# Optimization experiments

Hardware: AMD Instinct MI355X
Metric: run time of the kernel (lower is better)

The kernel has to match this reference:

```python
import jax, jax.numpy as jnp
import numpy as np

_SQRT4PI = float(np.sqrt(4.0 * np.pi))

def spherical_harmonics_l2(vec):
    # e3nn real spherical harmonics, lmax=2, normalize=True, normalization='integral'
    # component-normalized values divided by sqrt(4*pi); e3nn (x,y,z) ordering with y as zenith
    r = jnp.linalg.norm(vec, axis=-1, keepdims=True)
    u = vec / jnp.maximum(r, 1e-12)
    x, y, z = u[..., 0], u[..., 1], u[..., 2]
    c1 = np.float32(np.sqrt(3.0)); c2 = np.float32(np.sqrt(15.0)); c3 = np.float32(np.sqrt(5.0))
    sh = jnp.stack([
        jnp.ones_like(x),                      # l=0
        c1 * x, c1 * y, c1 * z,                # l=1
        c2 * x * z,                            # l=2
        c2 * x * y,
        c3 * (y * y - 0.5 * (x * x + z * z)),
        c2 * y * z,
        (c2 * 0.5) * (z * z - x * x),
    ], axis=-1)
    return sh * np.float32(1.0 / _SQRT4PI)

def setup_inputs() -> dict:
    key = jax.random.key(0)
    ks = jax.random.split(key, 8)
    N, M, C, F, SH = 50000, 12, 128, 64, 9
    return dict(
        atom_fea=jax.random.normal(ks[0], (N, C), jnp.float32),
        nbr_fea=jax.random.normal(ks[1], (N, M, F), jnp.float32),
        nbr_idx=jax.random.randint(ks[2], (N, M), 0, N),
        pos=jax.random.normal(ks[3], (N, 3), jnp.float32),
        w1=jax.random.normal(ks[4], (F, F), jnp.float32) * np.float32(1.0 / np.sqrt(F)),
        b1=jnp.zeros((F,), jnp.float32),
        w2=jax.random.normal(ks[5], (F, SH), jnp.float32) * np.float32(1.0 / np.sqrt(F)),
        b2=jnp.zeros((SH,), jnp.float32),
        tp_w=jax.random.normal(ks[6], (C, C), jnp.float32),  # FCTP weight, path (Cx0e)x(1x0e)->(Cx0e)
        bn_gamma=jnp.ones((C,), jnp.float32),
        bn_beta=jnp.zeros((C,), jnp.float32),
    )

def reference(atom_fea, nbr_fea, nbr_idx, pos, w1, b1, w2, b2, tp_w, bn_gamma, bn_beta):
    N, M, F = nbr_fea.shape
    C = atom_fea.shape[1]
    src = nbr_idx.reshape(-1)                                  # (E,)
    h_j = atom_fea[src]                                        # (E, C) gather
    # radial MLP: Linear -> Softplus -> Linear
    R = jax.nn.softplus(nbr_fea.reshape(N * M, F) @ w1 + b1) @ w2 + b2   # (E, 9)
    rel = pos[src] - jnp.repeat(pos, M, axis=0)                # (E, 3), dst = arange(N) repeated M times
    Y = spherical_harmonics_l2(rel)                            # (E, 9)
    W = R * Y                                                  # (E, 9)
    # FullyConnectedTensorProduct(Cx0e, 0e+1o+2e, Cx0e): only 0e x 0e -> 0e path survives,
    # fan-in normalization alpha = 1/sqrt(C)
    msg = (h_j @ tp_w) * W[:, :1] * np.float32(1.0 / np.sqrt(C))  # (E, C)
    # scatter-mean over dst: dst rows are contiguous blocks of size M per node
    agg = msg.reshape(N, M, C).mean(axis=1)                    # (N, C)
    x = atom_fea + agg
    # BatchNorm1d (training-mode batch statistics, eps=1e-5)
    mean = x.mean(axis=0)
    var = x.var(axis=0)
    xn = (x - mean) * jax.lax.rsqrt(var + 1e-5)
    return jax.nn.softplus(bn_gamma * xn + bn_beta)
```

## Files before the change

kernel.cpp:

```cpp
#include <hip/hip_runtime.h>
#include <hip/hip_bf16.h>
#include <cstddef>

#define N_NODES 50000
#define M_NBR   12
#define C_CH    128
#define F_DIM   64
#define E_EDGES (N_NODES * M_NBR)
#define NSUP    18750
#define NBLK_A  2344
#define NBLK_Y  782
#define NBLK_G  782

constexpr float SCALE_CE =
    (float)(1.0 / (3.5449077018110318 * 11.313708498984761 * 12.0));

typedef __bf16 bf16x8 __attribute__((ext_vector_type(8)));
typedef float  f32x4  __attribute__((ext_vector_type(4)));

__device__ __forceinline__ float softplus_f(float x) {
    const float t = __builtin_amdgcn_exp2f(-fabsf(x) * 1.44269504f);
    return fmaxf(x, 0.0f) + 0.69314718f * __builtin_amdgcn_logf(1.0f + t);
}

__device__ __forceinline__ float bfhi_to_f(unsigned int p) {
    return __uint_as_float(p & 0xffff0000u);
}
__device__ __forceinline__ float bflo_to_f(unsigned int p) {
    return __uint_as_float(p << 16);
}

__global__ __launch_bounds__(512) void kW(
    const float* __restrict__ w1,
    const float* __restrict__ tp_w,
    __bf16* __restrict__ fragW1,
    __bf16* __restrict__ fragTP)
{
    const int t = threadIdx.x;
    if (blockIdx.x == 0) {
        const int lane = t & 63;
        const int f = t >> 6;
        const int n = f >> 1, ks = f & 1;
        const int col16 = lane & 15, kgrp = lane >> 4;
        bf16x8 v;
        #pragma unroll
        for (int j = 0; j < 8; ++j)
            v[j] = (__bf16)w1[(ks * 32 + kgrp * 8 + j) * F_DIM + 16 * n + col16];
        *(bf16x8*)&fragW1[(size_t)t * 8] = v;
    } else {
        const int fid = (blockIdx.x - 1) * 512 + t;
        const int lane = fid & 63;
        const int f = fid >> 6;
        const int n = f >> 2, ks = f & 3;
        const int col16 = lane & 15, kgrp = lane >> 4;
        bf16x8 v;
        #pragma unroll
        for (int j = 0; j < 8; ++j)
            v[j] = (__bf16)tp_w[(ks * 32 + kgrp * 8 + j) * C_CH + 16 * n + col16];
        *(bf16x8*)&fragTP[(size_t)fid * 8] = v;
    }
}

__global__ __launch_bounds__(256) void kFront(
    const float* __restrict__ nbr_fea,
    const __bf16* __restrict__ fragW1,
    const float* __restrict__ b1,
    const float* __restrict__ w2,
    const float* __restrict__ b2,
    const float* __restrict__ atom_fea,
    const __bf16* __restrict__ fragTP,
    float* __restrict__ ce,
    __bf16* __restrict__ y)
{
    __shared__ __align__(16) unsigned char smem[4 * 32 * 272];
    const int tid   = threadIdx.x;
    const int lane  = tid & 63;
    const int wid   = tid >> 6;
    const int col16 = lane & 15;
    const int kgrp  = lane >> 4;

    if (blockIdx.x < NBLK_A) {
        bf16x8 bfrag[4][2];
        #pragma unroll
        for (int f = 0; f < 8; ++f)
            bfrag[f >> 1][f & 1] = *(const bf16x8*)&fragW1[((size_t)f * 64 + lane) * 8];

        float b1v[4], w2v[4];
        #pragma unroll
        for (int n = 0; n < 4; ++n) {
            b1v[n] = b1[16 * n + col16];
            w2v[n] = w2[(16 * n + col16) * 9];
        }
        const float b2_0 = b2[0];

        float* S = (float*)(smem + (size_t)wid * 32 * 272);
        const int sup_base = (blockIdx.x * 4 + wid) * 2;

        #pragma unroll
        for (int st = 0; st < 2; ++st) {
            const int sup = sup_base + st;
            if (sup >= NSUP) break;
            const long e0 = (long)sup * 32;
            const float* gsrc = nbr_fea + e0 * F_DIM;

            #pragma unroll
            for (int i = 0; i < 8; ++i) {
                const int gi16 = i * 64 + lane;
                const float4 v = *(const float4*)(gsrc + (size_t)gi16 * 4);
                const int row = gi16 >> 4;
                const int u   = gi16 & 15;
                *(float4*)(S + row * 68 + u * 4) = v;
            }

            #pragma unroll
            for (int t = 0; t < 2; ++t) {
                const float* R = S + (t * 16 + col16) * 68 + kgrp * 8;
                const float4 a0 = *(const float4*)(R);
                const float4 a1 = *(const float4*)(R + 4);
                const float4 a2 = *(const float4*)(R + 32);
                const float4 a3 = *(const float4*)(R + 36);

                bf16x8 afrag[2];
                afrag[0][0] = (__bf16)a0.x; afrag[0][1] = (__bf16)a0.y;
                afrag[0][2] = (__bf16)a0.z; afrag[0][3] = (__bf16)a0.w;
                afrag[0][4] = (__bf16)a1.x; afrag[0][5] = (__bf16)a1.y;
                afrag[0][6] = (__bf16)a1.z; afrag[0][7] = (__bf16)a1.w;
                afrag[1][0] = (__bf16)a2.x; afrag[1][1] = (__bf16)a2.y;
                afrag[1][2] = (__bf16)a2.z; afrag[1][3] = (__bf16)a2.w;
                afrag[1][4] = (__bf16)a3.x; afrag[1][5] = (__bf16)a3.y;
                afrag[1][6] = (__bf16)a3.z; afrag[1][7] = (__bf16)a3.w;

                f32x4 acc[4];
                #pragma unroll
                for (int n = 0; n < 4; ++n) acc[n] = (f32x4){0.f, 0.f, 0.f, 0.f};
                #pragma unroll
                for (int ks = 0; ks < 2; ++ks)
                    #pragma unroll
                    for (int n = 0; n < 4; ++n)
                        acc[n] = __builtin_amdgcn_mfma_f32_16x16x32_bf16(
                            afrag[ks], bfrag[n][ks], acc[n], 0, 0, 0);

                float partial[4] = {0.f, 0.f, 0.f, 0.f};
                #pragma unroll
                for (int n = 0; n < 4; ++n)
                    #pragma unroll
                    for (int r = 0; r < 4; ++r) {
                        const float h = acc[n][r] + b1v[n];
                        partial[r] = fmaf(softplus_f(h), w2v[n], partial[r]);
                    }
                #pragma unroll
                for (int r = 0; r < 4; ++r) {
                    #pragma unroll
                    for (int off = 1; off <= 8; off <<= 1)
                        partial[r] += __shfl_xor(partial[r], off);
                }
                if (col16 == 0) {
                    const long et = e0 + t * 16;
                    #pragma unroll
                    for (int r = 0; r < 4; ++r)
                        ce[et + kgrp * 4 + r] = (partial[r] + b2_0) * SCALE_CE;
                }
            }
        }
    } else {
        __bf16* yl = (__bf16*)smem;
        const int blk  = blockIdx.x - NBLK_A;
        const int row  = blk * 64 + wid * 16 + col16;
        const int rowc = row < N_NODES ? row : N_NODES - 1;
        const float* ap = atom_fea + (size_t)rowc * C_CH + kgrp * 8;

        bf16x8 afrag[4];
        #pragma unroll
        for (int ks = 0; ks < 4; ++ks) {
            float4 f0 = *(const float4*)(ap + ks * 32);
            float4 f1 = *(const float4*)(ap + ks * 32 + 4);
            afrag[ks][0] = (__bf16)f0.x; afrag[ks][1] = (__bf16)f0.y;
            afrag[ks][2] = (__bf16)f0.z; afrag[ks][3] = (__bf16)f0.w;
            afrag[ks][4] = (__bf16)f1.x; afrag[ks][5] = (__bf16)f1.y;
            afrag[ks][6] = (__bf16)f1.z; afrag[ks][7] = (__bf16)f1.w;
        }

        #pragma unroll
        for (int n = 0; n < 8; ++n) {
            f32x4 acc = (f32x4){0.f, 0.f, 0.f, 0.f};
            #pragma unroll
            for (int ks = 0; ks < 4; ++ks) {
                bf16x8 bf = *(const bf16x8*)&fragTP[((size_t)(n * 4 + ks) * 64 + lane) * 8];
                acc = __builtin_amdgcn_mfma_f32_16x16x32_bf16(afrag[ks], bf, acc, 0, 0, 0);
            }
            #pragma unroll
            for (int r = 0; r < 4; ++r)
                yl[(wid * 16 + kgrp * 4 + r) * 136 + 16 * n + col16] = (__bf16)acc[r];
        }
        __syncthreads();

        #pragma unroll
        for (int it = 0; it < 4; ++it) {
            const int e  = it * 2048 + tid * 8;
            const int rw = e >> 7, cl = e & 127;
            const int grow = blk * 64 + rw;
            if (grow < N_NODES) {
                bf16x8 v = *(const bf16x8*)&yl[rw * 136 + cl];
                *(bf16x8*)&y[(size_t)grow * C_CH + cl] = v;
            }
        }
    }
}

__global__ __launch_bounds__(256, 6) void kG(
    const float* __restrict__ atom_fea,
    const __bf16* __restrict__ y,
    const int*   __restrict__ nbr_idx,
    const float* __restrict__ ce,
    unsigned int* __restrict__ xb,
    float* __restrict__ psum,
    float* __restrict__ psumsq)
{
    __shared__ float4 red[4][64];
    const int tid  = threadIdx.x;
    const int lane = tid & 63;
    const int wid  = tid >> 6;
    const int blk  = blockIdx.x;
    const int i0   = blk * 64 + wid * 16;

    float2 sum   = make_float2(0.f, 0.f);
    float2 sumsq = make_float2(0.f, 0.f);

    int   pidx = 0;
    float pce  = 0.f;
    if (i0 < N_NODES && lane < M_NBR) {
        pidx = nbr_idx[i0 * M_NBR + lane];
        pce  = ce[i0 * M_NBR + lane];
    }

    for (int t = 0; t < 16; ++t) {
        const int i = i0 + t;
        const int   cidx = pidx;
        const float cce  = pce;
        const int inext = i + 1;
        if (t < 15 && inext < N_NODES && lane < M_NBR) {
            pidx = nbr_idx[inext * M_NBR + lane];
            pce  = ce[inext * M_NBR + lane];
        }
        if (i < N_NODES) {
            float2 acc = make_float2(0.f, 0.f);
            #pragma unroll
            for (int m = 0; m < M_NBR; ++m) {
                const int   src = __shfl(cidx, m);
                const float c   = __shfl(cce, m);
                const unsigned int p =
                    *(const unsigned int*)(y + (size_t)src * C_CH + lane * 2);
                acc.x = fmaf(c, bflo_to_f(p), acc.x);
                acc.y = fmaf(c, bfhi_to_f(p), acc.y);
            }
            const float2 a = *(const float2*)(atom_fea + (size_t)i * C_CH + lane * 2);
            const float2 xv = make_float2(a.x + acc.x, a.y + acc.y);
            union { __bf16 h[2]; unsigned int u; } pk;
            pk.h[0] = (__bf16)xv.x;
            pk.h[1] = (__bf16)xv.y;
            xb[(size_t)i * 64 + lane] = pk.u;
            sum.x += xv.x; sum.y += xv.y;
            sumsq.x += xv.x * xv.x; sumsq.y += xv.y * xv.y;
        }
    }

    red[wid][lane] = make_float4(sum.x, sum.y, sumsq.x, sumsq.y);
    __syncthreads();
    if (tid < 128) {
        const int l = tid >> 1, comp = tid & 1;
        float s = 0.f, q = 0.f;
        #pragma unroll
        for (int w = 0; w < 4; ++w) {
            const float4 v = red[w][l];
            s += comp ? v.y : v.x;
            q += comp ? v.w : v.z;
        }
        psum[blk * 128 + tid]   = s;
        psumsq[blk * 128 + tid] = q;
    }
}

__global__ __launch_bounds__(1024) void kC1(
    const float* __restrict__ psum,
    const float* __restrict__ psumsq,
    float* __restrict__ mean_o,
    float* __restrict__ istd_o,
    int nblocks)
{
    __shared__ float red[2][8][128];
    const int t = threadIdx.x;
    const int c = t & 127;
    const int grp = t >> 7;
    float s = 0.f, ss = 0.f;
    for (int b = grp; b < nblocks; b += 8) {
        s  += psum[b * 128 + c];
        ss += psumsq[b * 128 + c];
    }
    red[0][grp][c] = s;
    red[1][grp][c] = ss;
    __syncthreads();
    if (t < 128) {
        float S = 0.f, SS = 0.f;
        #pragma unroll
        for (int k = 0; k < 8; ++k) { S += red[0][k][t]; SS += red[1][k][t]; }
        const float m   = S / (float)N_NODES;
        const float var = SS / (float)N_NODES - m * m;
        mean_o[t] = m;
        istd_o[t] = rsqrtf(var + 1e-5f);
    }
}

__global__ __launch_bounds__(256) void kC2(
    const unsigned int* __restrict__ xb,
    float* __restrict__ out,
    const float* __restrict__ mean_i,
    const float* __restrict__ istd_i,
    const float* __restrict__ gamma,
    const float* __restrict__ beta)
{
    __shared__ float sm[128], si[128], sg[128], sb[128];
    const int tid = threadIdx.x;
    if (tid < 128) {
        sm[tid] = mean_i[tid];
        si[tid] = istd_i[tid];
        sg[tid] = gamma[tid];
        sb[tid] = beta[tid];
    }
    __syncthreads();
    const size_t tix = (size_t)blockIdx.x * 256 + tid;
    const uint2 v = *(const uint2*)&xb[tix * 2];
    const int c0 = (int)(tix & 31) * 4;
    float r[4] = {bflo_to_f(v.x), bfhi_to_f(v.x), bflo_to_f(v.y), bfhi_to_f(v.y)};
    float4 o;
    #pragma unroll
    for (int t = 0; t < 4; ++t) {
        const int cc = c0 + t;
        const float xn = (r[t] - sm[cc]) * si[cc];
        r[t] = softplus_f(fmaf(sg[cc], xn, sb[cc]));
    }
    o.x = r[0]; o.y = r[1]; o.z = r[2]; o.w = r[3];
    *(float4*)&out[tix * 4] = o;
}

extern "C" void kernel_launch(void* const* d_in, const int* in_sizes, int n_in,
                              void* d_out, int out_size, void* d_ws, size_t ws_size,
                              hipStream_t stream)
{
    const float* atom_fea = (const float*)d_in[0];
    const float* nbr_fea  = (const float*)d_in[1];
    const int*   nbr_idx  = (const int*)d_in[2];
    const float* w1       = (const float*)d_in[4];
    const float* b1       = (const float*)d_in[5];
    const float* w2       = (const float*)d_in[6];
    const float* b2       = (const float*)d_in[7];
    const float* tp_w     = (const float*)d_in[8];
    const float* bn_gamma = (const float*)d_in[9];
    const float* bn_beta  = (const float*)d_in[10];

    float* out = (float*)d_out;
    float* ws  = (float*)d_ws;

    float* ce      = ws;
    float* psum    = ce + E_EDGES;
    float* psumsq  = psum + (size_t)NBLK_G * 128;
    float* mean_b  = psumsq + (size_t)NBLK_G * 128;
    float* istd_b  = mean_b + 128;
    __bf16* fragW1 = (__bf16*)(istd_b + 128);
    __bf16* fragTP = fragW1 + 4096;
    __bf16* ybuf   = fragTP + 16384;
    unsigned int* xbuf = (unsigned int*)(ybuf + 6400000);

    kW<<<5, 512, 0, stream>>>(w1, tp_w, fragW1, fragTP);
    kFront<<<NBLK_A + NBLK_Y, 256, 0, stream>>>(
        nbr_fea, fragW1, b1, w2, b2, atom_fea, fragTP, ce, ybuf);
    kG<<<NBLK_G, 256, 0, stream>>>(atom_fea, ybuf, nbr_idx, ce,
                                   xbuf, psum, psumsq);
    kC1<<<1, 1024, 0, stream>>>(psum, psumsq, mean_b, istd_b, NBLK_G);
    const int nC2 = (N_NODES * C_CH / 4) / 256;
    kC2<<<nC2, 256, 0, stream>>>(xbuf, out, mean_b, istd_b, bn_gamma, bn_beta);
}
```

Measured before the change: 111.2 us.

## Prefetch nbr_fea in registers, stage bf16 in LDS, fuse BN reduction via last-block

The radial-MLP part of kFront now handles four 32-edge supertiles per wave and software-prefetches the next tile's nbr_fea into registers while the current one computes. Tiles are converted to bf16 before the LDS store, so A fragments become direct 16-byte vector loads and the LDS footprint shrinks. The separate kC1 reduction kernel is removed: kG uses an atomic counter with a last-block-done pattern to compute the batch-norm mean and inverse std, which saves one launch at the cost of a fence and an atomic per block. The counter is reset inside kFront, so correctness depends on stream ordering.

```diff
diff --git a/kernel.cpp b/kernel.cpp
--- a/kernel.cpp
+++ b/kernel.cpp
@@ -8,7 +8,8 @@
 #define F_DIM   64
 #define E_EDGES (N_NODES * M_NBR)
 #define NSUP    18750
-#define NBLK_A  2344
+#define SUP_PER_WAVE 4
+#define NBLK_A  1172
 #define NBLK_Y  782
 #define NBLK_G  782
 
@@ -70,15 +71,18 @@
     const float* __restrict__ atom_fea,
     const __bf16* __restrict__ fragTP,
     float* __restrict__ ce,
-    __bf16* __restrict__ y)
-{
-    __shared__ __align__(16) unsigned char smem[4 * 32 * 272];
+    __bf16* __restrict__ y,
+    unsigned int* __restrict__ counter)
+{
+    __shared__ __align__(16) unsigned char smem[18432];
     const int tid   = threadIdx.x;
     const int lane  = tid & 63;
     const int wid   = tid >> 6;
     const int col16 = lane & 15;
     const int kgrp  = lane >> 4;
 
+    if (blockIdx.x == 0 && tid == 0) *counter = 0;
+
     if (blockIdx.x < NBLK_A) {
         bf16x8 bfrag[4][2];
         #pragma unroll
@@ -93,42 +97,46 @@
         }
         const float b2_0 = b2[0];
 
-        float* S = (float*)(smem + (size_t)wid * 32 * 272);
-        const int sup_base = (blockIdx.x * 4 + wid) * 2;
-
-        #pragma unroll
-        for (int st = 0; st < 2; ++st) {
+        __bf16* S = (__bf16*)(smem + (size_t)wid * 4608);
+        const int sup_base = (blockIdx.x * 4 + wid) * SUP_PER_WAVE;
+
+        float4 pre[8];
+        if (sup_base < NSUP) {
+            const float* g = nbr_fea + (size_t)sup_base * 32 * F_DIM;
+            #pragma unroll
+            for (int i = 0; i < 8; ++i)
+                pre[i] = *(const float4*)(g + (size_t)(i * 64 + lane) * 4);
+        }
+
+        #pragma unroll
+        for (int st = 0; st < SUP_PER_WAVE; ++st) {
             const int sup = sup_base + st;
             if (sup >= NSUP) break;
-            const long e0 = (long)sup * 32;
-            const float* gsrc = nbr_fea + e0 * F_DIM;
 
             #pragma unroll
             for (int i = 0; i < 8; ++i) {
                 const int gi16 = i * 64 + lane;
-                const float4 v = *(const float4*)(gsrc + (size_t)gi16 * 4);
-                const int row = gi16 >> 4;
-                const int u   = gi16 & 15;
-                *(float4*)(S + row * 68 + u * 4) = v;
-            }
-
+                const int row = gi16 >> 4, u = gi16 & 15;
+                union { __bf16 h[4]; uint2 u2; } pk;
+                pk.h[0] = (__bf16)pre[i].x; pk.h[1] = (__bf16)pre[i].y;
+                pk.h[2] = (__bf16)pre[i].z; pk.h[3] = (__bf16)pre[i].w;
+                *(uint2*)&S[row * 72 + u * 4] = pk.u2;
+            }
+            if (st + 1 < SUP_PER_WAVE && sup + 1 < NSUP) {
+                const float* g = nbr_fea + (size_t)(sup + 1) * 32 * F_DIM;
+                #pragma unroll
+                for (int i = 0; i < 8; ++i)
+                    pre[i] = *(const float4*)(g + (size_t)(i * 64 + lane) * 4);
+            }
+
+            const long e0 = (long)sup * 32;
             #pragma unroll
             for (int t = 0; t < 2; ++t) {
-                const float* R = S + (t * 16 + col16) * 68 + kgrp * 8;
-                const float4 a0 = *(const float4*)(R);
-                const float4 a1 = *(const float4*)(R + 4);
-                const float4 a2 = *(const float4*)(R + 32);
-                const float4 a3 = *(const float4*)(R + 36);
-
                 bf16x8 afrag[2];
-                afrag[0][0] = (__bf16)a0.x; afrag[0][1] = (__bf16)a0.y;
-                afrag[0][2] = (__bf16)a0.z; afrag[0][3] = (__bf16)a0.w;
-                afrag[0][4] = (__bf16)a1.x; afrag[0][5] = (__bf16)a1.y;
-                afrag[0][6] = (__bf16)a1.z; afrag[0][7] = (__bf16)a1.w;
-                afrag[1][0] = (__bf16)a2.x; afrag[1][1] = (__bf16)a2.y;
-                afrag[1][2] = (__bf16)a2.z; afrag[1][3] = (__bf16)a2.w;
-                afrag[1][4] = (__bf16)a3.x; afrag[1][5] = (__bf16)a3.y;
-                afrag[1][6] = (__bf16)a3.z; afrag[1][7] = (__bf16)a3.w;
+                #pragma unroll
+                for (int ks = 0; ks < 2; ++ks)
+                    afrag[ks] = *(const bf16x8*)
+                        &S[(t * 16 + col16) * 72 + ks * 32 + kgrp * 8];
 
                 f32x4 acc[4];
                 #pragma unroll
@@ -214,9 +222,14 @@
     const float* __restrict__ ce,
     unsigned int* __restrict__ xb,
     float* __restrict__ psum,
-    float* __restrict__ psumsq)
+    float* __restrict__ psumsq,
+    float* __restrict__ mean_o,
+    float* __restrict__ istd_o,
+    unsigned int* __restrict__ counter)
 {
     __shared__ float4 red[4][64];
+    __shared__ float rs[2][2][128];
+    __shared__ int isLast;
     const int tid  = threadIdx.x;
     const int lane = tid & 63;
     const int wid  = tid >> 6;
@@ -278,35 +291,30 @@
         psum[blk * 128 + tid]   = s;
         psumsq[blk * 128 + tid] = q;
     }
-}
-
-__global__ __launch_bounds__(1024) void kC1(
-    const float* __restrict__ psum,
-    const float* __restrict__ psumsq,
-    float* __restrict__ mean_o,
-    float* __restrict__ istd_o,
-    int nblocks)
-{
-    __shared__ float red[2][8][128];
-    const int t = threadIdx.x;
-    const int c = t & 127;
-    const int grp = t >> 7;
-    float s = 0.f, ss = 0.f;
-    for (int b = grp; b < nblocks; b += 8) {
-        s  += psum[b * 128 + c];
-        ss += psumsq[b * 128 + c];
-    }
-    red[0][grp][c] = s;
-    red[1][grp][c] = ss;
+
+    __threadfence();
+    if (tid == 0)
+        isLast = (atomicAdd(counter, 1u) == (unsigned)(gridDim.x - 1));
     __syncthreads();
-    if (t < 128) {
-        float S = 0.f, SS = 0.f;
-        #pragma unroll
-        for (int k = 0; k < 8; ++k) { S += red[0][k][t]; SS += red[1][k][t]; }
-        const float m   = S / (float)N_NODES;
-        const float var = SS / (float)N_NODES - m * m;
-        mean_o[t] = m;
-        istd_o[t] = rsqrtf(var + 1e-5f);
+    if (isLast) {
+        __threadfence();
+        const int ch = tid & 127, half = tid >> 7;
+        float s = 0.f, q = 0.f;
+        for (int b = half; b < NBLK_G; b += 2) {
+            s += psum[b * 128 + ch];
+            q += psumsq[b * 128 + ch];
+        }
+        rs[0][half][ch] = s;
+        rs[1][half][ch] = q;
+        __syncthreads();
+        if (tid < 128) {
+            const float S  = rs[0][0][tid] + rs[0][1][tid];
+            const float SS = rs[1][0][tid] + rs[1][1][tid];
+            const float m   = S / (float)N_NODES;
+            const float var = SS / (float)N_NODES - m * m;
+            mean_o[tid] = m;
+            istd_o[tid] = rsqrtf(var + 1e-5f);
+        }
     }
 }
 
@@ -365,17 +373,17 @@
     float* psumsq  = psum + (size_t)NBLK_G * 128;
     float* mean_b  = psumsq + (size_t)NBLK_G * 128;
     float* istd_b  = mean_b + 128;
-    __bf16* fragW1 = (__bf16*)(istd_b + 128);
+    unsigned int* counter = (unsigned int*)(istd_b + 128);
+    __bf16* fragW1 = (__bf16*)(counter + 4);
     __bf16* fragTP = fragW1 + 4096;
     __bf16* ybuf   = fragTP + 16384;
     unsigned int* xbuf = (unsigned int*)(ybuf + 6400000);
 
     kW<<<5, 512, 0, stream>>>(w1, tp_w, fragW1, fragTP);
     kFront<<<NBLK_A + NBLK_Y, 256, 0, stream>>>(
-        nbr_fea, fragW1, b1, w2, b2, atom_fea, fragTP, ce, ybuf);
+        nbr_fea, fragW1, b1, w2, b2, atom_fea, fragTP, ce, ybuf, counter);
     kG<<<NBLK_G, 256, 0, stream>>>(atom_fea, ybuf, nbr_idx, ce,
-                                   xbuf, psum, psumsq);
-    kC1<<<1, 1024, 0, stream>>>(psum, psumsq, mean_b, istd_b, NBLK_G);
+                                   xbuf, psum, psumsq, mean_b, istd_b, counter);
     const int nC2 = (N_NODES * C_CH / 4) / 256;
     kC2<<<nC2, 256, 0, stream>>>(xbuf, out, mean_b, istd_b, bn_gamma, bn_beta);
 }
```

New measurement: 266.1 us. 139% more time.

## Prefetch next nbr_fea tile into registers and stage it in LDS as bf16

Applied to the files above, without the earlier changes.

Each wave now handles four 32-edge super-tiles instead of two, which halves the number of front blocks. The next tile's nbr_fea loads are issued into registers while the current tile is computed, so global latency overlaps with the MFMA work. The tile is converted to bf16 before the LDS write, which halves LDS footprint and lets A fragments be read as single 16-byte vector loads. The cost is more live registers and fewer blocks, which could reduce occupancy and latency hiding.

```diff
diff --git a/kernel.cpp b/kernel.cpp
--- a/kernel.cpp
+++ b/kernel.cpp
@@ -8,7 +8,8 @@
 #define F_DIM   64
 #define E_EDGES (N_NODES * M_NBR)
 #define NSUP    18750
-#define NBLK_A  2344
+#define SUP_PER_WAVE 4
+#define NBLK_A  1172
 #define NBLK_Y  782
 #define NBLK_G  782
 
@@ -72,7 +73,7 @@
     float* __restrict__ ce,
     __bf16* __restrict__ y)
 {
-    __shared__ __align__(16) unsigned char smem[4 * 32 * 272];
+    __shared__ __align__(16) unsigned char smem[18432];
     const int tid   = threadIdx.x;
     const int lane  = tid & 63;
     const int wid   = tid >> 6;
@@ -93,42 +94,46 @@
         }
         const float b2_0 = b2[0];
 
-        float* S = (float*)(smem + (size_t)wid * 32 * 272);
-        const int sup_base = (blockIdx.x * 4 + wid) * 2;
-
-        #pragma unroll
-        for (int st = 0; st < 2; ++st) {
+        __bf16* S = (__bf16*)(smem + (size_t)wid * 4608);
+        const int sup_base = (blockIdx.x * 4 + wid) * SUP_PER_WAVE;
+
+        float4 pre[8];
+        if (sup_base < NSUP) {
+            const float* g = nbr_fea + (size_t)sup_base * 32 * F_DIM;
+            #pragma unroll
+            for (int i = 0; i < 8; ++i)
+                pre[i] = *(const float4*)(g + (size_t)(i * 64 + lane) * 4);
+        }
+
+        #pragma unroll
+        for (int st = 0; st < SUP_PER_WAVE; ++st) {
             const int sup = sup_base + st;
             if (sup >= NSUP) break;
-            const long e0 = (long)sup * 32;
-            const float* gsrc = nbr_fea + e0 * F_DIM;
 
             #pragma unroll
             for (int i = 0; i < 8; ++i) {
                 const int gi16 = i * 64 + lane;
-                const float4 v = *(const float4*)(gsrc + (size_t)gi16 * 4);
-                const int row = gi16 >> 4;
-                const int u   = gi16 & 15;
-                *(float4*)(S + row * 68 + u * 4) = v;
-            }
-
+                const int row = gi16 >> 4, u = gi16 & 15;
+                union { __bf16 h[4]; uint2 u2; } pk;
+                pk.h[0] = (__bf16)pre[i].x; pk.h[1] = (__bf16)pre[i].y;
+                pk.h[2] = (__bf16)pre[i].z; pk.h[3] = (__bf16)pre[i].w;
+                *(uint2*)&S[row * 72 + u * 4] = pk.u2;
+            }
+            if (st + 1 < SUP_PER_WAVE && sup + 1 < NSUP) {
+                const float* g = nbr_fea + (size_t)(sup + 1) * 32 * F_DIM;
+                #pragma unroll
+                for (int i = 0; i < 8; ++i)
+                    pre[i] = *(const float4*)(g + (size_t)(i * 64 + lane) * 4);
+            }
+
+            const long e0 = (long)sup * 32;
             #pragma unroll
             for (int t = 0; t < 2; ++t) {
-                const float* R = S + (t * 16 + col16) * 68 + kgrp * 8;
-                const float4 a0 = *(const float4*)(R);
-                const float4 a1 = *(const float4*)(R + 4);
-                const float4 a2 = *(const float4*)(R + 32);
-                const float4 a3 = *(const float4*)(R + 36);
-
                 bf16x8 afrag[2];
-                afrag[0][0] = (__bf16)a0.x; afrag[0][1] = (__bf16)a0.y;
-                afrag[0][2] = (__bf16)a0.z; afrag[0][3] = (__bf16)a0.w;
-                afrag[0][4] = (__bf16)a1.x; afrag[0][5] = (__bf16)a1.y;
-                afrag[0][6] = (__bf16)a1.z; afrag[0][7] = (__bf16)a1.w;
-                afrag[1][0] = (__bf16)a2.x; afrag[1][1] = (__bf16)a2.y;
-                afrag[1][2] = (__bf16)a2.z; afrag[1][3] = (__bf16)a2.w;
-                afrag[1][4] = (__bf16)a3.x; afrag[1][5] = (__bf16)a3.y;
-                afrag[1][6] = (__bf16)a3.z; afrag[1][7] = (__bf16)a3.w;
+                #pragma unroll
+                for (int ks = 0; ks < 2; ++ks)
+                    afrag[ks] = *(const bf16x8*)
+                        &S[(t * 16 + col16) * 72 + ks * 32 + kgrp * 8];
 
                 f32x4 acc[4];
                 #pragma unroll
```

New measurement: 110.0 us, median of 2. About the same (-1.1%).
